# Performance work log

Hardware: AMD Instinct MI355X
Metric: run time of the kernel (lower is better)

The kernel has to match this reference:

```python
import jax, jax.numpy as jnp
import numpy as np

B, N, NFEAT, NHID1, NHID2 = 64, 1024, 512, 1024, 512


def setup_inputs() -> dict:
    key = jax.random.key(0)
    ks = jax.random.split(key, 9)
    stdv1 = 1.0 / np.sqrt(NHID1)
    stdv2 = 1.0 / np.sqrt(NHID2)
    stdvl = 1.0 / np.sqrt(NHID2)
    return {
        "x": jax.random.normal(ks[0], (B, N, NFEAT), dtype=jnp.float32),
        "adj": jax.random.uniform(ks[1], (B, N, N), dtype=jnp.float32),
        "length": jax.random.randint(ks[2], (B,), 1, N + 1, dtype=jnp.int32),
        "W1": jax.random.uniform(ks[3], (NFEAT, NHID1), jnp.float32, -stdv1, stdv1),
        "b1": jax.random.uniform(ks[4], (NHID1,), jnp.float32, -stdv1, stdv1),
        "W2": jax.random.uniform(ks[5], (NHID1, NHID2), jnp.float32, -stdv2, stdv2),
        "b2": jax.random.uniform(ks[6], (NHID2,), jnp.float32, -stdv2, stdv2),
        "Wl": jax.random.uniform(ks[7], (NHID2, 1), jnp.float32, -stdvl, stdvl),
        "bl": jax.random.uniform(ks[8], (1,), jnp.float32, -stdvl, stdvl),
    }


def _gc(x, adj, W, b):
    # support = x @ W per graph; output = adj @ support + b  (GraphConvolution)
    support = jnp.einsum("bnf,fh->bnh", x, W)
    return jnp.einsum("bnm,bmh->bnh", adj, support) + b


def reference(x, adj, length, W1, b1, W2, b2, Wl, bl):
    h = jax.nn.relu(_gc(x, adj, W1, b1))
    # dropout is identity in eval mode
    h = jax.nn.relu(_gc(h, adj, W2, b2))
    # ave_pooling: mean over first length[i] nodes
    mask = (jnp.arange(N)[None, :] < length[:, None]).astype(h.dtype)  # [B,N]
    pooled = jnp.einsum("bnh,bn->bh", h, mask) / length.astype(h.dtype)[:, None]
    return pooled @ Wl + bl  # [B,1]
```

## Files before the change

kernel.cpp:

```cpp
#include <hip/hip_runtime.h>
#include <hip/hip_bf16.h>
#include <stdint.h>


typedef short bf16x8 __attribute__((ext_vector_type(8)));
typedef short s16x4 __attribute__((ext_vector_type(4)));
typedef float f32x4 __attribute__((ext_vector_type(4)));

__device__ __forceinline__ unsigned short f2bf(float f) {
    union { float f; unsigned u; } v; v.f = f;
    unsigned r = v.u + 0x7fffu + ((v.u >> 16) & 1u);
    return (unsigned short)(r >> 16);
}
__device__ __forceinline__ float bf2f(unsigned short h) {
    union { unsigned u; float f; } v; v.u = ((unsigned)h) << 16;
    return v.f;
}

typedef const __attribute__((address_space(1))) void* gp1_t;
typedef __attribute__((address_space(3))) void* lp3_t;

__device__ __forceinline__ void ldsload16(const void* g, void* l) {
    __builtin_amdgcn_global_load_lds((gp1_t)(uintptr_t)g,
                                     (lp3_t)(unsigned)(uintptr_t)l,
                                     16, 0, 0);
}

#define BARF()   do { __builtin_amdgcn_s_barrier(); asm volatile("" ::: "memory"); } while (0)
#define LGKM0()  asm volatile("s_waitcnt lgkmcnt(0)" ::: "memory")
#define VMCNT4() asm volatile("s_waitcnt vmcnt(4)" ::: "memory")
#define VMCNT0() asm volatile("s_waitcnt vmcnt(0)" ::: "memory")
#define MFMA16(d, a, b) d = __builtin_amdgcn_mfma_f32_16x16x32_bf16(a, b, d, 0, 0, 0)

template<bool BIASRELU, bool SPLIT, bool ZSWZ, bool POOL>
__global__ __launch_bounds__(512, 1)
void gemm_nt8(const short* __restrict__ A, const short* __restrict__ B,
              short* __restrict__ C, const float* __restrict__ bias,
              int M, int N, int K,
              long long aStride, long long bStride, long long cStride,
              long long splitStride,
              const int* __restrict__ length, float* __restrict__ pool_out)
{
    __shared__ short sm[2][2][256 * 64];

    int bx, by, bz;
    if (ZSWZ) {
        const int P = gridDim.x * gridDim.y;
        const int f = blockIdx.x + gridDim.x * (blockIdx.y + gridDim.y * blockIdx.z);
        const int k = f & 7;
        const int j = f >> 3;
        const int zper = gridDim.z >> 3;
        const int jp = j / P;
        bz = k * zper + jp;
        const int rem = j - jp * P;
        bx = rem % gridDim.x;
        by = rem / gridDim.x;
    } else {
        bx = blockIdx.x; by = blockIdx.y; bz = blockIdx.z;
    }

    const int bM = by * 256;
    const int bN = bx * 256;
    const int z  = bz;

    int len = 0;
    if (POOL) {
        len = length[z];
        if (bM >= len) return;
    }

    const int tid  = threadIdx.x;
    const int wid  = tid >> 6;
    const int lane = tid & 63;
    const int wm   = wid >> 2;
    const int wn   = wid & 3;
    const int quad = lane >> 4;
    const int l16  = lane & 15;

    A += (long long)z * aStride;
    B += (long long)z * bStride;

    const int srow = tid >> 3;
    const int scbs = ((tid & 7) * 16) ^ ((srow & 7) << 4);
    const short* Ag = A + (long long)(bM + srow) * K + (scbs >> 1);
    const short* Bg = B + (long long)(bN + srow) * K + (scbs >> 1);
    const long long row64  = 64LL * K;
    const long long row128 = 128LL * K;

    #define STAGE(buf, ab, h, kt) do {                                        \
        const short* g_ = (ab ? Bg : Ag) + (h ? row128 : 0) + (kt) * 64;      \
        char* l_ = (char*)&sm[buf][ab][0] + (h) * 16384 + wid * 1024;         \
        ldsload16(g_, l_);                                                    \
        ldsload16(g_ + row64, l_ + 8192);                                     \
    } while (0)

    const int cbs0 = (quad * 16) ^ ((l16 & 7) << 4);
    const int cbs1 = (64 + quad * 16) ^ ((l16 & 7) << 4);

    #define RDA(buf, m, kk) (*(const bf16x8*)((const char*)&sm[buf][0][0]     \
        + (wm * 128 + (m) * 16 + l16) * 128 + ((kk) ? cbs1 : cbs0)))
    #define RDB(buf, n, kk) (*(const bf16x8*)((const char*)&sm[buf][1][0]     \
        + (wn * 64 + (n) * 16 + l16) * 128 + ((kk) ? cbs1 : cbs0)))

    f32x4 acc[8][4];
#pragma unroll
    for (int m = 0; m < 8; ++m) {
#pragma unroll
        for (int n = 0; n < 4; ++n) acc[m][n] = (f32x4)0.0f;
    }

    const int NT = K >> 6;

    STAGE(0, 0, 0, 0); STAGE(0, 0, 1, 0);
    STAGE(0, 1, 0, 0); STAGE(0, 1, 1, 0);
    STAGE(1, 1, 0, 1); STAGE(1, 0, 0, 1);
    VMCNT4();
    BARF();

    #define TILE_STEP(t, buf, bufn) do {                                      \
        int tn1 = (t) + 1; if (tn1 == NT) tn1 = 0;                            \
        int tn2 = (t) + 2; if (tn2 >= NT) tn2 -= NT;                          \
        bf16x8 a0[4], a1[4], p0[2], p1[2], q0[2], q1[2];                      \
             \
        _Pragma("unroll") for (int m = 0; m < 4; ++m) {                       \
            a0[m] = RDA(buf, m, 0); a1[m] = RDA(buf, m, 1); }                 \
        _Pragma("unroll") for (int n = 0; n < 2; ++n) {                       \
            p0[n] = RDB(buf, n, 0); p1[n] = RDB(buf, n, 1); }                 \
        STAGE(bufn, 0, 1, tn1);                                               \
        BARF(); LGKM0();                                                      \
        __builtin_amdgcn_s_setprio(1);                                        \
        _Pragma("unroll") for (int m = 0; m < 4; ++m) {                       \
            _Pragma("unroll") for (int n = 0; n < 2; ++n) {                   \
                MFMA16(acc[m][n], a0[m], p0[n]);                              \
                MFMA16(acc[m][n], a1[m], p1[n]); } }                          \
        __builtin_amdgcn_s_setprio(0);                                        \
        BARF();                                                               \
                       \
        _Pragma("unroll") for (int n = 0; n < 2; ++n) {                       \
            q0[n] = RDB(buf, 2 + n, 0); q1[n] = RDB(buf, 2 + n, 1); }         \
        STAGE(bufn, 1, 1, tn1);                                               \
        BARF(); LGKM0();                                                      \
        __builtin_amdgcn_s_setprio(1);                                        \
        _Pragma("unroll") for (int m = 0; m < 4; ++m) {                       \
            _Pragma("unroll") for (int n = 0; n < 2; ++n) {                   \
                MFMA16(acc[m][2 + n], a0[m], q0[n]);                          \
                MFMA16(acc[m][2 + n], a1[m], q1[n]); } }                      \
        __builtin_amdgcn_s_setprio(0);                                        \
        BARF();                                                               \
                       \
        _Pragma("unroll") for (int m = 0; m < 4; ++m) {                       \
            a0[m] = RDA(buf, 4 + m, 0); a1[m] = RDA(buf, 4 + m, 1); }         \
        STAGE(buf, 1, 0, tn2);                                                \
        BARF(); LGKM0();                                                      \
        __builtin_amdgcn_s_setprio(1);                                        \
        _Pragma("unroll") for (int m = 0; m < 4; ++m) {                       \
            _Pragma("unroll") for (int n = 0; n < 2; ++n) {                   \
                MFMA16(acc[4 + m][2 + n], a0[m], q0[n]);                      \
                MFMA16(acc[4 + m][2 + n], a1[m], q1[n]); } }                  \
        __builtin_amdgcn_s_setprio(0);                                        \
        BARF();                                                               \
           \
        STAGE(buf, 0, 0, tn2);                                                \
        BARF();                                                               \
        __builtin_amdgcn_s_setprio(1);                                        \
        _Pragma("unroll") for (int m = 0; m < 4; ++m) {                       \
            _Pragma("unroll") for (int n = 0; n < 2; ++n) {                   \
                MFMA16(acc[4 + m][n], a0[m], p0[n]);                          \
                MFMA16(acc[4 + m][n], a1[m], p1[n]); } }                      \
        __builtin_amdgcn_s_setprio(0);                                        \
        VMCNT4();      \
        BARF();                                                               \
    } while (0)

    for (int t = 0; t < NT; t += 2) {
        TILE_STEP(t, 0, 1);
        TILE_STEP(t + 1, 1, 0);
    }

    if (POOL) {
        VMCNT0();
        __syncthreads();
        float* red = (float*)&sm[0][0][0];
#pragma unroll
        for (int n = 0; n < 4; ++n) {
            const int col = wn * 64 + n * 16 + l16;
            const float bv = bias[bN + col];
            float cs = 0.0f;
#pragma unroll
            for (int m = 0; m < 8; ++m) {
                const int row0 = bM + wm * 128 + m * 16 + quad * 4;
#pragma unroll
                for (int r = 0; r < 4; ++r) {
                    const float val = fmaxf(acc[m][n][r] + bv, 0.0f);
                    if (row0 + r < len) cs += val;
                }
            }
            cs += __shfl_xor(cs, 16);
            cs += __shfl_xor(cs, 32);
            if (quad == 0) red[wm * 256 + col] = cs;
        }
        __syncthreads();
        if (tid < 256) {
            const float s = red[tid] + red[256 + tid];
            pool_out[((long long)z * 4 + by) * 512 + bN + tid] = s;
        }
        return;
    }

#pragma unroll
    for (int m = 0; m < 8; ++m) {
        const int row0 = bM + wm * 128 + m * 16 + quad * 4;
#pragma unroll
        for (int n = 0; n < 4; ++n) {
            const int col = bN + wn * 64 + n * 16 + l16;
            float bv = 0.0f;
            if (BIASRELU) bv = bias[col];
#pragma unroll
            for (int r = 0; r < 4; ++r) {
                float val = acc[m][n][r];
                if (BIASRELU) val = fmaxf(val + bv, 0.0f);
                long long addr;
                if (SPLIT) {
                    const int bb = col >> 10;
                    const int nn = col & 1023;
                    addr = (long long)bb * splitStride
                         + (long long)(row0 + r) * 1024 + nn;
                } else {
                    addr = (long long)z * cStride
                         + (long long)(row0 + r) * N + col;
                }
                C[addr] = (short)f2bf(val);
            }
        }
    }
    #undef TILE_STEP
    #undef STAGE
    #undef RDA
    #undef RDB
}

__global__ void cvt2_f32_bf16(const float4* __restrict__ inA, s16x4* __restrict__ outA, int nA4,
                              const float4* __restrict__ inB, s16x4* __restrict__ outB, int nB4)
{
    int i = blockIdx.x * 256 + threadIdx.x;
    const float4* in; s16x4* out; int j;
    if (i < nA4) { in = inA; out = outA; j = i; }
    else { j = i - nA4; if (j >= nB4) return; in = inB; out = outB; }
    float4 v = in[j];
    s16x4 o;
    o.x = (short)f2bf(v.x); o.y = (short)f2bf(v.y);
    o.z = (short)f2bf(v.z); o.w = (short)f2bf(v.w);
    out[j] = o;
}

__global__ void transpose_cvt(const float* __restrict__ in,
                              short* __restrict__ out, int R, int C)
{
    __shared__ float tile[32][33];
    const int bc = blockIdx.x * 32;
    const int br = blockIdx.y * 32;
    const int tx = threadIdx.x & 31;
    const int ty = threadIdx.x >> 5;
#pragma unroll
    for (int i = 0; i < 32; i += 8)
        tile[ty + i][tx] = in[(long long)(br + ty + i) * C + bc + tx];
    __syncthreads();
#pragma unroll
    for (int i = 0; i < 32; i += 8)
        out[(long long)(bc + ty + i) * R + br + tx] = (short)f2bf(tile[tx][ty + i]);
}

__global__ void pool_final3(const float* __restrict__ part,
                            const int* __restrict__ length,
                            const float* __restrict__ Wl,
                            const float* __restrict__ bl,
                            float* __restrict__ out)
{
    const int b = blockIdx.x;
    const int t = threadIdx.x;
    const int len = length[b];
    const int mbmax = (len + 255) >> 8;
    float s0 = 0.0f, s1 = 0.0f;
    for (int mb = 0; mb < mbmax; mb++) {
        float2 v = ((const float2*)part)[(b * 4 + mb) * 256 + t];
        s0 += v.x; s1 += v.y;
    }
    float v = s0 * Wl[2 * t] + s1 * Wl[2 * t + 1];
#pragma unroll
    for (int off = 32; off > 0; off >>= 1) v += __shfl_down(v, off);
    __shared__ float wsum[4];
    if ((t & 63) == 0) wsum[t >> 6] = v;
    __syncthreads();
    if (t == 0) {
        float s = wsum[0] + wsum[1] + wsum[2] + wsum[3];
        out[b] = s / (float)len + bl[0];
    }
}

extern "C" void kernel_launch(void* const* d_in, const int* in_sizes, int n_in,
                              void* d_out, int out_size, void* d_ws, size_t ws_size,
                              hipStream_t stream)
{
    const float* x    = (const float*)d_in[0];
    const float* adj  = (const float*)d_in[1];
    const int*   len  = (const int*)d_in[2];
    const float* W1   = (const float*)d_in[3];
    const float* b1   = (const float*)d_in[4];
    const float* W2   = (const float*)d_in[5];
    const float* b2   = (const float*)d_in[6];
    const float* Wl   = (const float*)d_in[7];
    const float* bl   = (const float*)d_in[8];
    float* out = (float*)d_out;

    char* ws = (char*)d_ws;
    short* adjB  = (short*)(ws);
    short* xS2T  = (short*)(ws + 134217728LL);
    short* W1T   = (short*)(ws + 201326592LL);
    short* W2T   = (short*)(ws + 202375168LL);
    short* S1T   = (short*)(ws + 203423744LL);
    short* h1    = (short*)(ws + 337641472LL);
    float* part  = (float*)(ws + 134217728LL + 33554432LL);

    cvt2_f32_bf16<<<98304, 256, 0, stream>>>(
        (const float4*)adj, (s16x4*)adjB, 16777216,
        (const float4*)x,   (s16x4*)xS2T,  8388608);
    transpose_cvt<<<dim3(32, 16), 256, 0, stream>>>(W1, W1T, 512, 1024);
    transpose_cvt<<<dim3(16, 32), 256, 0, stream>>>(W2, W2T, 1024, 512);

    gemm_nt8<false, true, false, false><<<dim3(256, 4, 1), 512, 0, stream>>>(
        W1T, xS2T, S1T, nullptr, 1024, 65536, 512, 0, 0, 0, 1048576LL, nullptr, nullptr);

    gemm_nt8<true, false, true, false><<<dim3(4, 4, 64), 512, 0, stream>>>(
        adjB, S1T, h1, b1, 1024, 1024, 1024, 1048576LL, 1048576LL, 1048576LL, 0, nullptr, nullptr);

    gemm_nt8<false, true, false, false><<<dim3(256, 2, 1), 512, 0, stream>>>(
        W2T, h1, xS2T, nullptr, 512, 65536, 1024, 0, 0, 0, 524288LL, nullptr, nullptr);

    gemm_nt8<true, false, true, true><<<dim3(2, 4, 64), 512, 0, stream>>>(
        adjB, xS2T, nullptr, b2, 1024, 512, 1024, 1048576LL, 524288LL, 0, 0, len, part);

    pool_final3<<<64, 256, 0, stream>>>(part, len, Wl, bl, out);
}
```

Measured before the change: 808.5 us.

## Fuse fp32-to-bf16 conversion of adj and x into GEMM tile loads

Removes the standalone conversion pass that wrote bf16 copies of adj and x. A new GEMM variant loads fp32 tiles straight into registers, packs them to bf16 and writes them to LDS, while the other operand still uses direct global-to-LDS loads. This avoids a full extra read and write of the large adjacency and feature tensors. In exchange the fp32 operand is read twice (once per adj GEMM), at double the bytes per element, with a shallower one-tile prefetch pipeline and extra VALU work for packing.

```diff
diff --git a/kernel.cpp b/kernel.cpp
--- a/kernel.cpp
+++ b/kernel.cpp
@@ -17,6 +17,15 @@
     return v.f;
 }
 
+__device__ __forceinline__ bf16x8 pack8(float4 a, float4 b) {
+    bf16x8 o;
+    o[0] = (short)f2bf(a.x); o[1] = (short)f2bf(a.y);
+    o[2] = (short)f2bf(a.z); o[3] = (short)f2bf(a.w);
+    o[4] = (short)f2bf(b.x); o[5] = (short)f2bf(b.y);
+    o[6] = (short)f2bf(b.z); o[7] = (short)f2bf(b.w);
+    return o;
+}
+
 typedef const __attribute__((address_space(1))) void* gp1_t;
 typedef __attribute__((address_space(3))) void* lp3_t;
 
@@ -28,8 +37,7 @@
 
 #define BARF()   do { __builtin_amdgcn_s_barrier(); asm volatile("" ::: "memory"); } while (0)
 #define LGKM0()  asm volatile("s_waitcnt lgkmcnt(0)" ::: "memory")
-#define VMCNT4() asm volatile("s_waitcnt vmcnt(4)" ::: "memory")
-#define VMCNT0() asm volatile("s_waitcnt vmcnt(0)" ::: "memory")
+#define VMCNT(n) asm volatile("s_waitcnt vmcnt(" #n ")" ::: "memory")
 #define MFMA16(d, a, b) d = __builtin_amdgcn_mfma_f32_16x16x32_bf16(a, b, d, 0, 0, 0)
 
 template<bool BIASRELU, bool SPLIT, bool ZSWZ, bool POOL>
@@ -114,14 +122,13 @@
     STAGE(0, 0, 0, 0); STAGE(0, 0, 1, 0);
     STAGE(0, 1, 0, 0); STAGE(0, 1, 1, 0);
     STAGE(1, 1, 0, 1); STAGE(1, 0, 0, 1);
-    VMCNT4();
+    VMCNT(4);
     BARF();
 
     #define TILE_STEP(t, buf, bufn) do {                                      \
         int tn1 = (t) + 1; if (tn1 == NT) tn1 = 0;                            \
         int tn2 = (t) + 2; if (tn2 >= NT) tn2 -= NT;                          \
         bf16x8 a0[4], a1[4], p0[2], p1[2], q0[2], q1[2];                      \
-             \
         _Pragma("unroll") for (int m = 0; m < 4; ++m) {                       \
             a0[m] = RDA(buf, m, 0); a1[m] = RDA(buf, m, 1); }                 \
         _Pragma("unroll") for (int n = 0; n < 2; ++n) {                       \
@@ -135,7 +142,6 @@
                 MFMA16(acc[m][n], a1[m], p1[n]); } }                          \
         __builtin_amdgcn_s_setprio(0);                                        \
         BARF();                                                               \
-                       \
         _Pragma("unroll") for (int n = 0; n < 2; ++n) {                       \
             q0[n] = RDB(buf, 2 + n, 0); q1[n] = RDB(buf, 2 + n, 1); }         \
         STAGE(bufn, 1, 1, tn1);                                               \
@@ -147,7 +153,6 @@
                 MFMA16(acc[m][2 + n], a1[m], q1[n]); } }                      \
         __builtin_amdgcn_s_setprio(0);                                        \
         BARF();                                                               \
-                       \
         _Pragma("unroll") for (int m = 0; m < 4; ++m) {                       \
             a0[m] = RDA(buf, 4 + m, 0); a1[m] = RDA(buf, 4 + m, 1); }         \
         STAGE(buf, 1, 0, tn2);                                                \
@@ -159,7 +164,6 @@
                 MFMA16(acc[4 + m][2 + n], a1[m], q1[n]); } }                  \
         __builtin_amdgcn_s_setprio(0);                                        \
         BARF();                                                               \
-           \
         STAGE(buf, 0, 0, tn2);                                                \
         BARF();                                                               \
         __builtin_amdgcn_s_setprio(1);                                        \
@@ -168,7 +172,7 @@
                 MFMA16(acc[4 + m][n], a0[m], p0[n]);                          \
                 MFMA16(acc[4 + m][n], a1[m], p1[n]); } }                      \
         __builtin_amdgcn_s_setprio(0);                                        \
-        VMCNT4();      \
+        VMCNT(4);                                                             \
         BARF();                                                               \
     } while (0)
 
@@ -178,7 +182,7 @@
     }
 
     if (POOL) {
-        VMCNT0();
+        VMCNT(0);
         __syncthreads();
         float* red = (float*)&sm[0][0][0];
 #pragma unroll
@@ -239,18 +243,238 @@
     #undef RDB
 }
 
-__global__ void cvt2_f32_bf16(const float4* __restrict__ inA, s16x4* __restrict__ outA, int nA4,
-                              const float4* __restrict__ inB, s16x4* __restrict__ outB, int nB4)
+template<bool BIASRELU, bool SPLIT, bool ZSWZ, bool POOL, int FPS>
+__global__ __launch_bounds__(512, 2)
+void gemm_ntf(const short* __restrict__ Xbf, const float* __restrict__ Xfp,
+              short* __restrict__ C, const float* __restrict__ bias,
+              int M, int N, int K,
+              long long bfStride, long long fpStride, long long cStride,
+              long long splitStride,
+              const int* __restrict__ length, float* __restrict__ pool_out)
 {
-    int i = blockIdx.x * 256 + threadIdx.x;
-    const float4* in; s16x4* out; int j;
-    if (i < nA4) { in = inA; out = outA; j = i; }
-    else { j = i - nA4; if (j >= nB4) return; in = inB; out = outB; }
-    float4 v = in[j];
-    s16x4 o;
-    o.x = (short)f2bf(v.x); o.y = (short)f2bf(v.y);
-    o.z = (short)f2bf(v.z); o.w = (short)f2bf(v.w);
-    out[j] = o;
+    __shared__ short sm[2][2][256 * 64];
+
+    int bx, by, bz;
+    if (ZSWZ) {
+        const int P = gridDim.x * gridDim.y;
+        const int f = blockIdx.x + gridDim.x * (blockIdx.y + gridDim.y * blockIdx.z);
+        const int k = f & 7;
+        const int j = f >> 3;
+        const int zper = gridDim.z >> 3;
+        const int jp = j / P;
+        bz = k * zper + jp;
+        const int rem = j - jp * P;
+        bx = rem % gridDim.x;
+        by = rem / gridDim.x;
+    } else {
+        bx = blockIdx.x; by = blockIdx.y; bz = blockIdx.z;
+    }
+
+    const int bM = by * 256;
+    const int bN = bx * 256;
+    const int z  = bz;
+
+    int len = 0;
+    if (POOL) {
+        len = length[z];
+        if (bM >= len) return;
+    }
+
+    const int tid  = threadIdx.x;
+    const int wid  = tid >> 6;
+    const int lane = tid & 63;
+    const int wm   = wid >> 2;
+    const int wn   = wid & 3;
+    const int quad = lane >> 4;
+    const int l16  = lane & 15;
+
+    constexpr int FP_SIDE = FPS;
+    constexpr int GL_SIDE = 1 - FPS;
+
+    const int fpRow0 = (FPS == 0) ? bM : bN;
+    const int glRow0 = (FPS == 0) ? bN : bM;
+
+    const int srow = tid >> 3;
+    const int scbs = ((tid & 7) * 16) ^ ((srow & 7) << 4);
+    const short* Gbf = Xbf + (long long)z * bfStride
+                     + (long long)(glRow0 + srow) * K + (scbs >> 1);
+    const float* Gfp = Xfp + (long long)z * fpStride
+                     + (long long)(fpRow0 + srow) * K + (scbs >> 1);
+    const long long r64s  = 64LL * K;
+    const long long r128s = 128LL * K;
+    const long long r64f  = 64LL * K;
+    const long long r128f = 128LL * K;
+
+    #define GLDSF(buf, h, kt) do {                                            \
+        const short* g_ = Gbf + ((h) ? r128s : 0) + (long long)(kt) * 64;     \
+        char* l_ = (char*)&sm[buf][GL_SIDE][0] + (h) * 16384 + wid * 1024;    \
+        ldsload16(g_, l_);                                                    \
+        ldsload16(g_ + r64s, l_ + 8192);                                      \
+    } while (0)
+
+    #define FPISSUE(h, kt, ra, rb, rc, rd) do {                               \
+        const float* f_ = Gfp + ((h) ? r128f : 0) + (long long)(kt) * 64;     \
+        ra = *(const float4*)f_;       rb = *(const float4*)(f_ + 4);         \
+        rc = *(const float4*)(f_ + r64f); rd = *(const float4*)(f_ + r64f + 4); \
+    } while (0)
+
+    #define FPWRITE(buf, h, ra, rb, rc, rd) do {                              \
+        char* d_ = (char*)&sm[buf][FP_SIDE][0] + (h) * 16384 + tid * 16;      \
+        *(bf16x8*)d_          = pack8(ra, rb);                                \
+        *(bf16x8*)(d_ + 8192) = pack8(rc, rd);                                \
+    } while (0)
+
+    const int cbs0 = (quad * 16) ^ ((l16 & 7) << 4);
+    const int cbs1 = (64 + quad * 16) ^ ((l16 & 7) << 4);
+
+    #define RDAF(buf, m, kk) (*(const bf16x8*)((const char*)&sm[buf][0][0]    \
+        + (wm * 128 + (m) * 16 + l16) * 128 + ((kk) ? cbs1 : cbs0)))
+    #define RDBF(buf, n, kk) (*(const bf16x8*)((const char*)&sm[buf][1][0]    \
+        + (wn * 64 + (n) * 16 + l16) * 128 + ((kk) ? cbs1 : cbs0)))
+
+    #define MFMAQ(MO, NO, AA0, AA1, XX0, XX1)                                 \
+        _Pragma("unroll") for (int m_ = 0; m_ < 4; ++m_) {                    \
+            _Pragma("unroll") for (int n_ = 0; n_ < 2; ++n_) {                \
+                MFMA16(acc[(MO) + m_][(NO) + n_], AA0[m_], XX0[n_]);          \
+                MFMA16(acc[(MO) + m_][(NO) + n_], AA1[m_], XX1[n_]); } }
+
+    f32x4 acc[8][4];
+#pragma unroll
+    for (int m = 0; m < 8; ++m) {
+#pragma unroll
+        for (int n = 0; n < 4; ++n) acc[m][n] = (f32x4)0.0f;
+    }
+
+    const int NT = K >> 6;
+
+    {
+        float4 pa, pb, pc, pd, pe, pf, pg, ph;
+        FPISSUE(0, 0, pa, pb, pc, pd);
+        FPISSUE(1, 0, pe, pf, pg, ph);
+        GLDSF(0, 0, 0); GLDSF(0, 1, 0);
+        VMCNT(8);
+        FPWRITE(0, 0, pa, pb, pc, pd);
+        VMCNT(4);
+        FPWRITE(0, 1, pe, pf, pg, ph);
+        asm volatile("s_waitcnt vmcnt(0) lgkmcnt(0)" ::: "memory");
+        BARF();
+    }
+
+    #define TSTEPF(t, CUR, NXT) do {                                          \
+        int tn = (t) + 1; if (tn == NT) tn = 0;                               \
+        bf16x8 a0[4], a1[4], p0[2], p1[2], q0[2], q1[2];                      \
+        float4 fa, fb, fc, fd, fe, ff, fg, fh;                                \
+                                                                     \
+        _Pragma("unroll") for (int m = 0; m < 4; ++m) {                       \
+            a0[m] = RDAF(CUR, m, 0); a1[m] = RDAF(CUR, m, 1); }               \
+        _Pragma("unroll") for (int n = 0; n < 2; ++n) {                       \
+            p0[n] = RDBF(CUR, n, 0); p1[n] = RDBF(CUR, n, 1); }               \
+        FPISSUE(0, tn, fa, fb, fc, fd);                                       \
+        GLDSF(NXT, 0, tn);                                                    \
+        BARF(); LGKM0();                                                      \
+        __builtin_amdgcn_s_setprio(1);                                        \
+        MFMAQ(0, 0, a0, a1, p0, p1);                                          \
+        __builtin_amdgcn_s_setprio(0);                                        \
+        BARF();                                                               \
+                                                                     \
+        _Pragma("unroll") for (int n = 0; n < 2; ++n) {                       \
+            q0[n] = RDBF(CUR, 2 + n, 0); q1[n] = RDBF(CUR, 2 + n, 1); }       \
+        FPISSUE(1, tn, fe, ff, fg, fh);                                       \
+        GLDSF(NXT, 1, tn);                                                    \
+        BARF(); LGKM0();                                                      \
+        __builtin_amdgcn_s_setprio(1);                                        \
+        MFMAQ(0, 2, a0, a1, q0, q1);                                          \
+        __builtin_amdgcn_s_setprio(0);                                        \
+        BARF();                                                               \
+                                                                     \
+        _Pragma("unroll") for (int m = 0; m < 4; ++m) {                       \
+            a0[m] = RDAF(CUR, 4 + m, 0); a1[m] = RDAF(CUR, 4 + m, 1); }       \
+        VMCNT(8);                                                             \
+        FPWRITE(NXT, 0, fa, fb, fc, fd);                                      \
+        BARF(); LGKM0();                                                      \
+        __builtin_amdgcn_s_setprio(1);                                        \
+        MFMAQ(4, 2, a0, a1, q0, q1);                                          \
+        __builtin_amdgcn_s_setprio(0);                                        \
+        BARF();                                                               \
+                                                                     \
+        VMCNT(2);                                                             \
+        FPWRITE(NXT, 1, fe, ff, fg, fh);                                      \
+        BARF(); LGKM0();                                                      \
+        __builtin_amdgcn_s_setprio(1);                                        \
+        MFMAQ(4, 0, a0, a1, p0, p1);                                          \
+        __builtin_amdgcn_s_setprio(0);                                        \
+        VMCNT(0);                                                             \
+        BARF();                                                               \
+    } while (0)
+
+    for (int t = 0; t < NT; t += 2) {
+        TSTEPF(t, 0, 1);
+        TSTEPF(t + 1, 1, 0);
+    }
+
+    if (POOL) {
+        VMCNT(0);
+        __syncthreads();
+        float* red = (float*)&sm[0][0][0];
+#pragma unroll
+        for (int n = 0; n < 4; ++n) {
+            const int col = wn * 64 + n * 16 + l16;
+            const float bv = bias[bN + col];
+            float cs = 0.0f;
+#pragma unroll
+            for (int m = 0; m < 8; ++m) {
+                const int row0 = bM + wm * 128 + m * 16 + quad * 4;
+#pragma unroll
+                for (int r = 0; r < 4; ++r) {
+                    const float val = fmaxf(acc[m][n][r] + bv, 0.0f);
+                    if (row0 + r < len) cs += val;
+                }
+            }
+            cs += __shfl_xor(cs, 16);
+            cs += __shfl_xor(cs, 32);
+            if (quad == 0) red[wm * 256 + col] = cs;
+        }
+        __syncthreads();
+        if (tid < 256) {
+            const float s = red[tid] + red[256 + tid];
+            pool_out[((long long)z * 4 + by) * 512 + bN + tid] = s;
+        }
+        return;
+    }
+
+#pragma unroll
+    for (int m = 0; m < 8; ++m) {
+        const int row0 = bM + wm * 128 + m * 16 + quad * 4;
+#pragma unroll
+        for (int n = 0; n < 4; ++n) {
+            const int col = bN + wn * 64 + n * 16 + l16;
+            float bv = 0.0f;
+            if (BIASRELU) bv = bias[col];
+#pragma unroll
+            for (int r = 0; r < 4; ++r) {
+                float val = acc[m][n][r];
+                if (BIASRELU) val = fmaxf(val + bv, 0.0f);
+                long long addr;
+                if (SPLIT) {
+                    const int bb = col >> 10;
+                    const int nn = col & 1023;
+                    addr = (long long)bb * splitStride
+                         + (long long)(row0 + r) * 1024 + nn;
+                } else {
+                    addr = (long long)z * cStride
+                         + (long long)(row0 + r) * N + col;
+                }
+                C[addr] = (short)f2bf(val);
+            }
+        }
+    }
+    #undef TSTEPF
+    #undef GLDSF
+    #undef FPISSUE
+    #undef FPWRITE
+    #undef RDAF
+    #undef RDBF
+    #undef MFMAQ
 }
 
 __global__ void transpose_cvt(const float* __restrict__ in,
@@ -313,31 +537,27 @@
     float* out = (float*)d_out;
 
     char* ws = (char*)d_ws;
-    short* adjB  = (short*)(ws);
-    short* xS2T  = (short*)(ws + 134217728LL);
-    short* W1T   = (short*)(ws + 201326592LL);
-    short* W2T   = (short*)(ws + 202375168LL);
-    short* S1T   = (short*)(ws + 203423744LL);
-    short* h1    = (short*)(ws + 337641472LL);
-    float* part  = (float*)(ws + 134217728LL + 33554432LL);
-
-    cvt2_f32_bf16<<<98304, 256, 0, stream>>>(
-        (const float4*)adj, (s16x4*)adjB, 16777216,
-        (const float4*)x,   (s16x4*)xS2T,  8388608);
+    short* W1T  = (short*)(ws);
+    short* W2T  = (short*)(ws + 1048576LL);
+    float* part = (float*)(ws + 2097152LL);
+    short* S1T  = (short*)(ws + 16777216LL);
+    short* h1   = (short*)(ws + 150994944LL);
+    short* S2T  = (short*)(ws + 285212672LL);
+
     transpose_cvt<<<dim3(32, 16), 256, 0, stream>>>(W1, W1T, 512, 1024);
     transpose_cvt<<<dim3(16, 32), 256, 0, stream>>>(W2, W2T, 1024, 512);
 
-    gemm_nt8<false, true, false, false><<<dim3(256, 4, 1), 512, 0, stream>>>(
-        W1T, xS2T, S1T, nullptr, 1024, 65536, 512, 0, 0, 0, 1048576LL, nullptr, nullptr);
-
-    gemm_nt8<true, false, true, false><<<dim3(4, 4, 64), 512, 0, stream>>>(
-        adjB, S1T, h1, b1, 1024, 1024, 1024, 1048576LL, 1048576LL, 1048576LL, 0, nullptr, nullptr);
+    gemm_ntf<false, true, false, false, 1><<<dim3(256, 4, 1), 512, 0, stream>>>(
+        W1T, x, S1T, nullptr, 1024, 65536, 512, 0, 0, 0, 1048576LL, nullptr, nullptr);
+
+    gemm_ntf<true, false, true, false, 0><<<dim3(4, 4, 64), 512, 0, stream>>>(
+        S1T, adj, h1, b1, 1024, 1024, 1024, 1048576LL, 1048576LL, 1048576LL, 0, nullptr, nullptr);
 
     gemm_nt8<false, true, false, false><<<dim3(256, 2, 1), 512, 0, stream>>>(
-        W2T, h1, xS2T, nullptr, 512, 65536, 1024, 0, 0, 0, 524288LL, nullptr, nullptr);
-
-    gemm_nt8<true, false, true, true><<<dim3(2, 4, 64), 512, 0, stream>>>(
-        adjB, xS2T, nullptr, b2, 1024, 512, 1024, 1048576LL, 524288LL, 0, 0, len, part);
+        W2T, h1, S2T, nullptr, 512, 65536, 1024, 0, 0, 0, 524288LL, nullptr, nullptr);
+
+    gemm_ntf<true, false, true, true, 0><<<dim3(2, 4, 64), 512, 0, stream>>>(
+        S2T, adj, nullptr, b2, 1024, 512, 1024, 524288LL, 1048576LL, 0, 0, len, part);
 
     pool_final3<<<64, 256, 0, stream>>>(part, len, Wl, bl, out);
 }
```

Result: slower. 946.0 us (+17.0%).
